# Kernel tuning notes

Hardware: AMD Instinct MI355X
Metric: run time of the kernel (lower is better)

## Reference

```python
import jax, jax.numpy as jnp
import numpy as np

DIM = 1024
SEQ = 4096


def setup_inputs() -> dict:
    key = jax.random.key(0)
    ks = jax.random.split(key, 7)
    s = 1.0 / np.sqrt(DIM)
    return {
        "X": jax.random.normal(ks[0], (SEQ, DIM), dtype=jnp.float32),
        "Wq": jax.random.uniform(ks[1], (DIM, DIM), jnp.float32, -s, s),
        "bq": jax.random.uniform(ks[2], (DIM,), jnp.float32, -s, s),
        "Wk": jax.random.uniform(ks[3], (DIM, DIM), jnp.float32, -s, s),
        "bk": jax.random.uniform(ks[4], (DIM,), jnp.float32, -s, s),
        "Wv": jax.random.uniform(ks[5], (DIM, DIM), jnp.float32, -s, s),
        "bv": jax.random.uniform(ks[6], (DIM,), jnp.float32, -s, s),
    }


def reference(X, Wq, bq, Wk, bk, Wv, bv):
    # QKV projections (nn.Linear: x @ W.T + b); here W stored as [in, out]
    Q = X @ Wq + bq            # [S, D]
    K = X @ Wk + bk            # [S, D]
    V = X @ Wv + bv            # [S, D]
    scale = 1.0 / jnp.sqrt(jnp.asarray(X.shape[-1], X.dtype))
    scores = (Q @ K.T) * scale  # [S, S]
    attn = jax.nn.softmax(scores, axis=-1)
    return attn @ V            # [S, D]
```

## Files before the change

kernel.cpp:

```cpp
#include <hip/hip_runtime.h>

typedef unsigned short u16;
typedef unsigned int u32;
typedef __bf16 bf16x8 __attribute__((ext_vector_type(8)));
typedef float f32x4 __attribute__((ext_vector_type(4)));
typedef u16 u16x4 __attribute__((ext_vector_type(4)));

__device__ __forceinline__ u16 f32_to_bf16(float f) {
    u32 u = __builtin_bit_cast(u32, f);
    u32 r = (u + 0x7fffu + ((u >> 16) & 1u)) >> 16;
    return (u16)r;
}

__device__ __forceinline__ void async_cp16(const u16* g, u16* l) {
    __builtin_amdgcn_global_load_lds(
        (const __attribute__((address_space(1))) u32*)g,
        (__attribute__((address_space(3))) u32*)l, 16, 0, 0);
}

#define GEMM_PROLOG(Aptr, Bptr, LDA, LDB)                                     \
    __shared__ u16 lds[16384];                                                \
    const int tid  = threadIdx.x;                                             \
    const int wid  = tid >> 6;                                                \
    const int lane = tid & 63;                                                \
    const int s0 = wid * 2, s1 = s0 + 1;                                      \
    const int rr = lane >> 2;                                                 \
    const int cc = (lane & 3) * 8;                                            \
    const u16* gA0 = (Aptr) + (size_t)(bm + s0 * 16 + rr) * (LDA) + cc;       \
    const u16* gA1 = (Aptr) + (size_t)(bm + s1 * 16 + rr) * (LDA) + cc;       \
    const u16* gB0 = (Bptr) + (size_t)(bn + s0 * 16 + rr) * (LDB) + cc;       \
    const u16* gB1 = (Bptr) + (size_t)(bn + s1 * 16 + rr) * (LDB) + cc;       \
    u16* lA0  = &lds[s0 * 512];                                               \
    u16* lA1  = &lds[s1 * 512];                                               \
    u16* lB0  = &lds[4096 + s0 * 512];                                        \
    u16* lB1  = &lds[4096 + s1 * 512];                                        \
    const int wm = (wid >> 1) * 64;                                           \
    const int wn = (wid & 1) * 64;                                            \
    const int row16 = lane & 15;                                              \
    const int quad  = lane >> 4;                                              \
    f32x4 acc[4][4];                                                          \
    const f32x4 zero = {0.f, 0.f, 0.f, 0.f};                                  \
    _Pragma("unroll")                                                         \
    for (int i = 0; i < 4; i++)                                               \
        _Pragma("unroll")                                                     \
        for (int j = 0; j < 4; j++) acc[i][j] = zero;

#define GEMM_KLOOP(KLEN)                                                      \
    {                                                                         \
        async_cp16(gA0, lA0);                                                 \
        async_cp16(gA1, lA1);                                                 \
        async_cp16(gB0, lB0);                                                 \
        async_cp16(gB1, lB1);                                                 \
        gA0 += 32; gA1 += 32; gB0 += 32; gB1 += 32;                           \
        const int NIT = (KLEN) >> 5;                                          \
        for (int it = 0; it < NIT; ++it) {                                    \
            const int cur = (it & 1) << 13;       \
            const int nxt = 8192 - cur;                                       \
            __syncthreads();       \
            if (it + 1 < NIT) {                                               \
                async_cp16(gA0, lA0 + nxt);                                   \
                async_cp16(gA1, lA1 + nxt);                                   \
                async_cp16(gB0, lB0 + nxt);                                   \
                async_cp16(gB1, lB1 + nxt);                                   \
                gA0 += 32; gA1 += 32; gB0 += 32; gB1 += 32;                   \
            }                                                                 \
            bf16x8 fa[4], fb[4];                                              \
            _Pragma("unroll")                                                 \
            for (int im = 0; im < 4; im++)                                    \
                fa[im] = *(const bf16x8*)&lds[cur + (wm + im * 16 + row16) * 32 + quad * 8]; \
            _Pragma("unroll")                                                 \
            for (int in = 0; in < 4; in++)                                    \
                fb[in] = *(const bf16x8*)&lds[cur + 4096 + (wn + in * 16 + row16) * 32 + quad * 8]; \
            _Pragma("unroll")                                                 \
            for (int im = 0; im < 4; im++)                                    \
                _Pragma("unroll")                                             \
                for (int in = 0; in < 4; in++)                                \
                    acc[im][in] = __builtin_amdgcn_mfma_f32_16x16x32_bf16(    \
                        fa[im], fb[in], acc[im][in], 0, 0, 0);                \
        }                                                                     \
    }

#define SWIZZLE_2D()                                                          \
    const int L   = blockIdx.x;                                               \
    const int id2 = L & 255;                                                  \
    const int bm  = (((id2 & 7) * 4) + (id2 >> 6)) * 128;                     \
    const int bn  = (((id2 >> 3) & 7) + (L >> 8) * 8) * 128;

__global__ __launch_bounds__(256, 4)
void gemm_qkv(const u16* __restrict__ A, const u16* __restrict__ B,
              u16* __restrict__ C, u16* __restrict__ Vt,
              const float* __restrict__ bias,
              int K, int lda, int ldb, int ldc)
{
    SWIZZLE_2D()
    GEMM_PROLOG(A, B, lda, ldb)
    GEMM_KLOOP(K)
    if (bn < 2048) {
        #pragma unroll
        for (int im = 0; im < 4; im++) {
            #pragma unroll
            for (int in = 0; in < 4; in++) {
                const int n = bn + wn + in * 16 + row16;
                const float bv = bias[n];
                #pragma unroll
                for (int r = 0; r < 4; r++) {
                    const int m = bm + wm + im * 16 + quad * 4 + r;
                    C[(size_t)m * ldc + n] = f32_to_bf16(acc[im][in][r] + bv);
                }
            }
        }
    } else {
        #pragma unroll
        for (int im = 0; im < 4; im++) {
            #pragma unroll
            for (int in = 0; in < 4; in++) {
                const int n = bn + wn + in * 16 + row16;
                const float bv = bias[n];
                const int d = n - 2048;
                const int m = bm + wm + im * 16 + quad * 4;
                u16x4 pk;
                #pragma unroll
                for (int r = 0; r < 4; r++)
                    pk[r] = f32_to_bf16(acc[im][in][r] + bv);
                *(u16x4*)&Vt[(size_t)d * 4096 + m] = pk;
            }
        }
    }
}

__global__ __launch_bounds__(256, 4)
void gemm_score_exp(const u16* __restrict__ A, const u16* __restrict__ B,
                    u16* __restrict__ P, float* __restrict__ rowsum,
                    int K, int lda, int ldb, int ldc, float scale)
{
    SWIZZLE_2D()
    GEMM_PROLOG(A, B, lda, ldb)
    GEMM_KLOOP(K)
    #pragma unroll
    for (int im = 0; im < 4; im++) {
        #pragma unroll
        for (int r = 0; r < 4; r++) {
            const int m = bm + wm + im * 16 + quad * 4 + r;
            float rs = 0.f;
            #pragma unroll
            for (int in = 0; in < 4; in++) {
                const int n = bn + wn + in * 16 + row16;
                float e = __expf(acc[im][in][r] * scale);
                P[(size_t)m * ldc + n] = f32_to_bf16(e);
                rs += e;
            }
            rs += __shfl_xor(rs, 1);
            rs += __shfl_xor(rs, 2);
            rs += __shfl_xor(rs, 4);
            rs += __shfl_xor(rs, 8);
            if (row16 == 0) atomicAdd(&rowsum[m], rs);
        }
    }
}

__global__ __launch_bounds__(256, 4)
void gemm_pv_splitk(const u16* __restrict__ A, const u16* __restrict__ B,
                    float* __restrict__ C0, float* __restrict__ C1,
                    float* __restrict__ C2, float* __restrict__ C3,
                    int Kq, int lda, int ldb, int ldc)
{
    const int id2 = blockIdx.x;
    const int bm  = (((id2 & 7) * 4) + (id2 >> 6)) * 128;
    const int bn  = ((id2 >> 3) & 7) * 128;
    const int z   = blockIdx.y;
    float* C = (z == 0) ? C0 : (z == 1) ? C1 : (z == 2) ? C2 : C3;
    const int koff = z * Kq;
    GEMM_PROLOG(A + koff, B + koff, lda, ldb)
    GEMM_KLOOP(Kq)
    #pragma unroll
    for (int im = 0; im < 4; im++) {
        #pragma unroll
        for (int in = 0; in < 4; in++) {
            const int n = bn + wn + in * 16 + row16;
            #pragma unroll
            for (int r = 0; r < 4; r++) {
                const int m = bm + wm + im * 16 + quad * 4 + r;
                C[(size_t)m * ldc + n] = acc[im][in][r];
            }
        }
    }
}

__global__ __launch_bounds__(256)
void reduce4_scale(float4* __restrict__ out, const float4* __restrict__ p1,
                   const float4* __restrict__ p2, const float4* __restrict__ p3,
                   const float* __restrict__ rowsum)
{
    const int i = blockIdx.x * 256 + threadIdx.x;
    const float inv = 1.0f / rowsum[i >> 8];
    float4 a = out[i], b = p1[i], c = p2[i], d = p3[i];
    a.x = (a.x + b.x + c.x + d.x) * inv;
    a.y = (a.y + b.y + c.y + d.y) * inv;
    a.z = (a.z + b.z + c.z + d.z) * inv;
    a.w = (a.w + b.w + c.w + d.w) * inv;
    out[i] = a;
}

__global__ __launch_bounds__(256)
void prep_all(const float4* __restrict__ X, uint2* __restrict__ Xb,
              const float* __restrict__ W0, const float* __restrict__ W1,
              const float* __restrict__ W2, u16* __restrict__ Wt,
              const float* __restrict__ bq, const float* __restrict__ bk,
              const float* __restrict__ bv, float* __restrict__ b3,
              float* __restrict__ rowsum)
{
    __shared__ float t[32][33];
    const int b = blockIdx.x;
    if (b < 4096) {
        const int i = b * 256 + threadIdx.x;
        float4 v = X[i];
        uint2 o;
        o.x = (u32)f32_to_bf16(v.x) | ((u32)f32_to_bf16(v.y) << 16);
        o.y = (u32)f32_to_bf16(v.z) | ((u32)f32_to_bf16(v.w) << 16);
        Xb[i] = o;
    } else if (b < 7168) {
        const int tt = b - 4096;
        const int z  = tt >> 10;
        const int r  = tt & 1023;
        const float* W = (z == 0) ? W0 : (z == 1) ? W1 : W2;
        u16* dst = Wt + (size_t)z * 1024 * 1024;
        const int bk2 = (r & 31) * 32;
        const int bn2 = (r >> 5) * 32;
        const int tx = threadIdx.x & 31;
        const int ty = threadIdx.x >> 5;
        #pragma unroll
        for (int i = 0; i < 32; i += 8)
            t[ty + i][tx] = W[(size_t)(bk2 + ty + i) * 1024 + bn2 + tx];
        __syncthreads();
        #pragma unroll
        for (int i = 0; i < 32; i += 8)
            dst[(size_t)(bn2 + ty + i) * 1024 + bk2 + tx] = f32_to_bf16(t[tx][ty + i]);
    } else {
        const int i = (b - 7168) * 256 + threadIdx.x;
        if (i < 3072)
            b3[i] = (i < 1024) ? bq[i] : (i < 2048) ? bk[i - 1024] : bv[i - 2048];
        else
            rowsum[i - 3072] = 0.f;
    }
}

extern "C" void kernel_launch(void* const* d_in, const int* in_sizes, int n_in,
                              void* d_out, int out_size, void* d_ws, size_t ws_size,
                              hipStream_t stream)
{
    const float* X  = (const float*)d_in[0];
    const float* Wq = (const float*)d_in[1];
    const float* bq = (const float*)d_in[2];
    const float* Wk = (const float*)d_in[3];
    const float* bk = (const float*)d_in[4];
    const float* Wv = (const float*)d_in[5];
    const float* bv = (const float*)d_in[6];
    float* out = (float*)d_out;

    char* ws = (char*)d_ws;
    u16*   P      = (u16*)ws;
    u16*   Xb     = (u16*)ws;
    u16*   WqkvT  = (u16*)(ws + (8u << 20));
    float* rowsum = (float*)(ws + (32u << 20));
    float* bias3  = (float*)(ws + (32u << 20) + (64u << 10));
    u16*   QKV    = (u16*)(ws + (33u << 20));
    float* p1     = (float*)(ws + (33u << 20));
    float* p2     = (float*)(ws + (49u << 20));
    float* p3     = (float*)(ws + (65u << 20));
    u16*   Vt     = (u16*)(ws + (82u << 20));

    prep_all<<<7196, 256, 0, stream>>>((const float4*)X, (uint2*)Xb,
        Wq, Wk, Wv, WqkvT, bq, bk, bv, bias3, rowsum);

    gemm_qkv<<<768, 256, 0, stream>>>(Xb, WqkvT, QKV, Vt, bias3,
        1024, 1024, 1024, 3072);

    gemm_score_exp<<<1024, 256, 0, stream>>>(QKV, QKV + 1024, P, rowsum,
        1024, 3072, 3072, 4096, 0.03125f);

    gemm_pv_splitk<<<dim3(256, 4), 256, 0, stream>>>(P, Vt, out, p1, p2, p3,
        1024, 4096, 4096, 1024);

    reduce4_scale<<<4096, 256, 0, stream>>>((float4*)out, (const float4*)p1,
        (const float4*)p2, (const float4*)p3, rowsum);
}
```

Before: 218.2 us.

## Replace double-buffered K32 pipeline with single-buffered K64 steps; store split-K partials as bf16

```diff
diff --git a/kernel.cpp b/kernel.cpp
--- a/kernel.cpp
+++ b/kernel.cpp
@@ -10,6 +10,11 @@
     u32 u = __builtin_bit_cast(u32, f);
     u32 r = (u + 0x7fffu + ((u >> 16) & 1u)) >> 16;
     return (u16)r;
+}
+
+__device__ __forceinline__ float bf16_to_f32(u16 h) {
+    u32 u = (u32)h << 16;
+    return __builtin_bit_cast(float, u);
 }
 
 __device__ __forceinline__ void async_cp16(const u16* g, u16* l) {
@@ -27,13 +32,17 @@
     const int rr = lane >> 2;                                                 \
     const int cc = (lane & 3) * 8;                                            \
     const u16* gA0 = (Aptr) + (size_t)(bm + s0 * 16 + rr) * (LDA) + cc;       \
-    const u16* gA1 = (Aptr) + (size_t)(bm + s1 * 16 + rr) * (LDA) + cc;       \
+    const u16* gA1 = (Aptr) + (size_t)(bm + s1 * 16 + rr) * (LDA) + cc;      \
     const u16* gB0 = (Bptr) + (size_t)(bn + s0 * 16 + rr) * (LDB) + cc;       \
     const u16* gB1 = (Bptr) + (size_t)(bn + s1 * 16 + rr) * (LDB) + cc;       \
     u16* lA0  = &lds[s0 * 512];                                               \
     u16* lA1  = &lds[s1 * 512];                                               \
-    u16* lB0  = &lds[4096 + s0 * 512];                                        \
-    u16* lB1  = &lds[4096 + s1 * 512];                                        \
+    u16* lA0h = lA0 + 4096;                                                   \
+    u16* lA1h = lA1 + 4096;                                                   \
+    u16* lB0  = &lds[8192 + s0 * 512];                                        \
+    u16* lB1  = &lds[8192 + s1 * 512];                                        \
+    u16* lB0h = lB0 + 4096;                                                   \
+    u16* lB1h = lB1 + 4096;                                                   \
     const int wm = (wid >> 1) * 64;                                           \
     const int wn = (wid & 1) * 64;                                            \
     const int row16 = lane & 15;                                              \
@@ -46,31 +55,27 @@
         for (int j = 0; j < 4; j++) acc[i][j] = zero;
 
 #define GEMM_KLOOP(KLEN)                                                      \
-    {                                                                         \
+    for (int kt = 0; kt < (KLEN); kt += 64) {                                 \
+        __syncthreads();                                                      \
         async_cp16(gA0, lA0);                                                 \
         async_cp16(gA1, lA1);                                                 \
+        async_cp16(gA0 + 32, lA0h);                                           \
+        async_cp16(gA1 + 32, lA1h);                                           \
         async_cp16(gB0, lB0);                                                 \
         async_cp16(gB1, lB1);                                                 \
-        gA0 += 32; gA1 += 32; gB0 += 32; gB1 += 32;                           \
-        const int NIT = (KLEN) >> 5;                                          \
-        for (int it = 0; it < NIT; ++it) {                                    \
-            const int cur = (it & 1) << 13;       \
-            const int nxt = 8192 - cur;                                       \
-            __syncthreads();       \
-            if (it + 1 < NIT) {                                               \
-                async_cp16(gA0, lA0 + nxt);                                   \
-                async_cp16(gA1, lA1 + nxt);                                   \
-                async_cp16(gB0, lB0 + nxt);                                   \
-                async_cp16(gB1, lB1 + nxt);                                   \
-                gA0 += 32; gA1 += 32; gB0 += 32; gB1 += 32;                   \
-            }                                                                 \
+        async_cp16(gB0 + 32, lB0h);                                           \
+        async_cp16(gB1 + 32, lB1h);                                           \
+        gA0 += 64; gA1 += 64; gB0 += 64; gB1 += 64;                           \
+        __syncthreads();                                                      \
+        _Pragma("unroll")                                                     \
+        for (int h = 0; h < 2; h++) {                                         \
             bf16x8 fa[4], fb[4];                                              \
             _Pragma("unroll")                                                 \
             for (int im = 0; im < 4; im++)                                    \
-                fa[im] = *(const bf16x8*)&lds[cur + (wm + im * 16 + row16) * 32 + quad * 8]; \
+                fa[im] = *(const bf16x8*)&lds[h * 4096 + (wm + im * 16 + row16) * 32 + quad * 8]; \
             _Pragma("unroll")                                                 \
             for (int in = 0; in < 4; in++)                                    \
-                fb[in] = *(const bf16x8*)&lds[cur + 4096 + (wn + in * 16 + row16) * 32 + quad * 8]; \
+                fb[in] = *(const bf16x8*)&lds[8192 + h * 4096 + (wn + in * 16 + row16) * 32 + quad * 8]; \
             _Pragma("unroll")                                                 \
             for (int im = 0; im < 4; im++)                                    \
                 _Pragma("unroll")                                             \
@@ -160,15 +165,15 @@
 
 __global__ __launch_bounds__(256, 4)
 void gemm_pv_splitk(const u16* __restrict__ A, const u16* __restrict__ B,
-                    float* __restrict__ C0, float* __restrict__ C1,
-                    float* __restrict__ C2, float* __restrict__ C3,
+                    u16* __restrict__ P0, u16* __restrict__ P1,
+                    u16* __restrict__ P2, u16* __restrict__ P3,
                     int Kq, int lda, int ldb, int ldc)
 {
     const int id2 = blockIdx.x;
     const int bm  = (((id2 & 7) * 4) + (id2 >> 6)) * 128;
     const int bn  = ((id2 >> 3) & 7) * 128;
     const int z   = blockIdx.y;
-    float* C = (z == 0) ? C0 : (z == 1) ? C1 : (z == 2) ? C2 : C3;
+    u16* C = (z == 0) ? P0 : (z == 1) ? P1 : (z == 2) ? P2 : P3;
     const int koff = z * Kq;
     GEMM_PROLOG(A + koff, B + koff, lda, ldb)
     GEMM_KLOOP(Kq)
@@ -180,25 +185,26 @@
             #pragma unroll
             for (int r = 0; r < 4; r++) {
                 const int m = bm + wm + im * 16 + quad * 4 + r;
-                C[(size_t)m * ldc + n] = acc[im][in][r];
+                C[(size_t)m * ldc + n] = f32_to_bf16(acc[im][in][r]);
             }
         }
     }
 }
 
 __global__ __launch_bounds__(256)
-void reduce4_scale(float4* __restrict__ out, const float4* __restrict__ p1,
-                   const float4* __restrict__ p2, const float4* __restrict__ p3,
-                   const float* __restrict__ rowsum)
+void reduce4_scale(float4* __restrict__ out, const u16x4* __restrict__ p0,
+                   const u16x4* __restrict__ p1, const u16x4* __restrict__ p2,
+                   const u16x4* __restrict__ p3, const float* __restrict__ rowsum)
 {
     const int i = blockIdx.x * 256 + threadIdx.x;
     const float inv = 1.0f / rowsum[i >> 8];
-    float4 a = out[i], b = p1[i], c = p2[i], d = p3[i];
-    a.x = (a.x + b.x + c.x + d.x) * inv;
-    a.y = (a.y + b.y + c.y + d.y) * inv;
-    a.z = (a.z + b.z + c.z + d.z) * inv;
-    a.w = (a.w + b.w + c.w + d.w) * inv;
-    out[i] = a;
+    u16x4 a = p0[i], b = p1[i], c = p2[i], d = p3[i];
+    float4 o;
+    o.x = (bf16_to_f32(a[0]) + bf16_to_f32(b[0]) + bf16_to_f32(c[0]) + bf16_to_f32(d[0])) * inv;
+    o.y = (bf16_to_f32(a[1]) + bf16_to_f32(b[1]) + bf16_to_f32(c[1]) + bf16_to_f32(d[1])) * inv;
+    o.z = (bf16_to_f32(a[2]) + bf16_to_f32(b[2]) + bf16_to_f32(c[2]) + bf16_to_f32(d[2])) * inv;
+    o.w = (bf16_to_f32(a[3]) + bf16_to_f32(b[3]) + bf16_to_f32(c[3]) + bf16_to_f32(d[3])) * inv;
+    out[i] = o;
 }
 
 __global__ __launch_bounds__(256)
@@ -264,10 +270,11 @@
     float* rowsum = (float*)(ws + (32u << 20));
     float* bias3  = (float*)(ws + (32u << 20) + (64u << 10));
     u16*   QKV    = (u16*)(ws + (33u << 20));
-    float* p1     = (float*)(ws + (33u << 20));
-    float* p2     = (float*)(ws + (49u << 20));
-    float* p3     = (float*)(ws + (65u << 20));
-    u16*   Vt     = (u16*)(ws + (82u << 20));
+    u16*   p0     = (u16*)(ws + (33u << 20));
+    u16*   p1     = (u16*)(ws + (41u << 20));
+    u16*   p2     = (u16*)(ws + (49u << 20));
+    u16*   p3     = (u16*)(ws + (57u << 20));
+    u16*   Vt     = (u16*)(ws + (65u << 20));
 
     prep_all<<<7196, 256, 0, stream>>>((const float4*)X, (uint2*)Xb,
         Wq, Wk, Wv, WqkvT, bq, bk, bv, bias3, rowsum);
@@ -278,9 +285,9 @@
     gemm_score_exp<<<1024, 256, 0, stream>>>(QKV, QKV + 1024, P, rowsum,
         1024, 3072, 3072, 4096, 0.03125f);
 
-    gemm_pv_splitk<<<dim3(256, 4), 256, 0, stream>>>(P, Vt, out, p1, p2, p3,
+    gemm_pv_splitk<<<dim3(256, 4), 256, 0, stream>>>(P, Vt, p0, p1, p2, p3,
         1024, 4096, 4096, 1024);
 
-    reduce4_scale<<<4096, 256, 0, stream>>>((float4*)out, (const float4*)p1,
-        (const float4*)p2, (const float4*)p3, rowsum);
-}
+    reduce4_scale<<<4096, 256, 0, stream>>>((float4*)out, (const u16x4*)p0,
+        (const u16x4*)p1, (const u16x4*)p2, (const u16x4*)p3, rowsum);
+}
```

Result: faster. 202.0 us (-7.4%).
